# Kernel optimization log

Measured on AMD Instinct MI355X. Metric: run time of the kernel, lower is better.

## Reference

```python
import jax, jax.numpy as jnp
import numpy as np

D, H, K, L, F, G, M, OUT = 1280, 16, 80, 4, 5120, 48, 2, 2048
HALF = K // 2  # rotary half dim = 40


def _token_coords(grid_thw, merge_size, N):
    tpi = grid_thw[:, 0] * grid_thw[:, 1] * grid_thw[:, 2]
    cu = jnp.concatenate([jnp.zeros(1, jnp.int32), jnp.cumsum(tpi).astype(jnp.int32)])
    tok = jnp.arange(N, dtype=jnp.int32)
    img_id = jnp.searchsorted(cu[1:], tok, side='right')
    local = tok - cu[img_id]
    h = grid_thw[img_id, 1]
    w = grid_thw[img_id, 2]
    spatial = local % (h * w)
    msq = merge_size * merge_size
    mw = w // merge_size
    group, intra = spatial // msq, spatial % msq
    row = (group // mw) * merge_size + intra // merge_size
    col = (group % mw) * merge_size + intra % merge_size
    return row, col, h, w, cu


def _layernorm(x, s, b, eps=1e-6):
    mu = jnp.mean(x, -1, keepdims=True)
    var = jnp.mean(jnp.square(x - mu), -1, keepdims=True)
    return (x - mu) * jax.lax.rsqrt(var + eps) * s + b


def _rotate_half(x):
    x1, x2 = x[..., :HALF], x[..., HALF:]
    return jnp.concatenate([-x2, x1], axis=-1)


def setup_inputs() -> dict:
    key = jax.random.key(0)
    ks = jax.random.split(key, 16)
    s = 0.02
    inp = {
        'pixels': jax.random.normal(ks[0], (2048, 1536), jnp.float32),
        'grid_thw': jnp.array([[1, 16, 32]] * 4, jnp.int32),
        'pos_embed': jax.random.normal(ks[1], (G * G, D), jnp.float32) * s,
        'patch_w': jax.random.normal(ks[2], (1536, D), jnp.float32) * s,
        'patch_b': jnp.zeros((D,), jnp.float32),
        'ln1_s': jnp.ones((L, D), jnp.float32), 'ln1_b': jnp.zeros((L, D), jnp.float32),
        'qkv_w': jax.random.normal(ks[3], (L, D, 3 * D), jnp.float32) * s,
        'qkv_b': jnp.zeros((L, 3 * D), jnp.float32),
        'proj_w': jax.random.normal(ks[4], (L, D, D), jnp.float32) * s,
        'proj_b': jnp.zeros((L, D), jnp.float32),
        'ln2_s': jnp.ones((L, D), jnp.float32), 'ln2_b': jnp.zeros((L, D), jnp.float32),
        'fc1_w': jax.random.normal(ks[5], (L, D, F), jnp.float32) * s,
        'fc1_b': jnp.zeros((L, F), jnp.float32),
        'fc2_w': jax.random.normal(ks[6], (L, F, D), jnp.float32) * s,
        'fc2_b': jnp.zeros((L, D), jnp.float32),
        'm_norm_s': jnp.ones((D,), jnp.float32), 'm_norm_b': jnp.zeros((D,), jnp.float32),
        'm_fc1_w': jax.random.normal(ks[7], (D * M * M, D * M * M), jnp.float32) * s,
        'm_fc1_b': jnp.zeros((D * M * M,), jnp.float32),
        'm_fc2_w': jax.random.normal(ks[8], (D * M * M, OUT), jnp.float32) * s,
        'm_fc2_b': jnp.zeros((OUT,), jnp.float32),
    }
    return inp


def _forward(pixels, grid_thw, pos_embed, patch_w, patch_b, ln1_s, ln1_b, qkv_w, qkv_b,
             proj_w, proj_b, ln2_s, ln2_b, fc1_w, fc1_b, fc2_w, fc2_b,
             m_norm_s, m_norm_b, m_fc1_w, m_fc1_b, m_fc2_w, m_fc2_b):
    N = pixels.shape[0]
    row, col, h, w, cu = _token_coords(grid_thw, M, N)

    # patch embed: conv with stride==kernel over flattened patches == linear
    x = pixels @ patch_w + patch_b  # [N, D]

    # bilinear position-embedding interpolation onto each image's (h, w) grid
    rf = jnp.where(h > 1, row.astype(jnp.float32) * (G - 1) / jnp.maximum(h - 1, 1), 0.0)
    cf = jnp.where(w > 1, col.astype(jnp.float32) * (G - 1) / jnp.maximum(w - 1, 1), 0.0)
    r0 = jnp.floor(rf).astype(jnp.int32); r1 = jnp.minimum(r0 + 1, G - 1)
    c0 = jnp.floor(cf).astype(jnp.int32); c1 = jnp.minimum(c0 + 1, G - 1)
    wr = (rf - r0)[:, None]; wc = (cf - c0)[:, None]
    pe = (pos_embed[r0 * G + c0] * (1 - wr) * (1 - wc)
          + pos_embed[r0 * G + c1] * (1 - wr) * wc
          + pos_embed[r1 * G + c0] * wr * (1 - wc)
          + pos_embed[r1 * G + c1] * wr * wc)
    x = x + pe

    # 2-D rotary embeddings
    inv_freq = 1.0 / (10000.0 ** (jnp.arange(0, HALF, 2, dtype=jnp.float32) / HALF))
    freqs = jnp.concatenate([row[:, None].astype(jnp.float32) * inv_freq,
                             col[:, None].astype(jnp.float32) * inv_freq], axis=-1)  # [N, HALF]
    emb = jnp.concatenate([freqs, freqs], axis=-1)  # [N, K]
    cos, sin = jnp.cos(emb)[:, None, :], jnp.sin(emb)[:, None, :]  # [N,1,K]

    # block-diagonal segment mask via cu_seqlens (N is a multiple of 128; no pad)
    tok = jnp.arange(N)
    seg = jnp.searchsorted(cu[1:], tok, side='right')
    k_start = cu[jnp.minimum(seg, cu.shape[0] - 2)]
    k_end = cu[jnp.minimum(seg + 1, cu.shape[0] - 1)]
    mask = (tok[None, :] >= k_start[:, None]) & (tok[None, :] < k_end[:, None])  # [N,N]
    scale = K ** -0.5

    for l in range(L):
        hdn = _layernorm(x, ln1_s[l], ln1_b[l])
        qkv = (hdn @ qkv_w[l] + qkv_b[l]).reshape(N, 3, H, K)
        q, k, v = qkv[:, 0], qkv[:, 1], qkv[:, 2]
        q = q * cos + _rotate_half(q) * sin
        k = k * cos + _rotate_half(k) * sin
        scores = jnp.einsum('nhk,mhk->hnm', q, k) * scale
        scores = jnp.where(mask[None], scores, jnp.finfo(scores.dtype).min)
        attn = jax.nn.softmax(scores, axis=-1)
        o = jnp.einsum('hnm,mhk->nhk', attn, v).reshape(N, D)
        x = x + o @ proj_w[l] + proj_b[l]

        hdn = _layernorm(x, ln2_s[l], ln2_b[l])
        ff = jax.nn.gelu(hdn @ fc1_w[l] + fc1_b[l], approximate=True)
        x = x + ff @ fc2_w[l] + fc2_b[l]

    # patch merger
    normed = _layernorm(x, m_norm_s, m_norm_b).reshape(N // (M * M), D * M * M)
    ff = jax.nn.gelu(normed @ m_fc1_w + m_fc1_b, approximate=True)
    return ff @ m_fc2_w + m_fc2_b  # [N/4, OUT]


def reference(pixels, grid_thw, pos_embed, patch_w, patch_b, ln1_s, ln1_b, qkv_w, qkv_b,
              proj_w, proj_b, ln2_s, ln2_b, fc1_w, fc1_b, fc2_w, fc2_b,
              m_norm_s, m_norm_b, m_fc1_w, m_fc1_b, m_fc2_w, m_fc2_b):
    return _forward(pixels, grid_thw, pos_embed, patch_w, patch_b, ln1_s, ln1_b, qkv_w, qkv_b,
                    proj_w, proj_b, ln2_s, ln2_b, fc1_w, fc1_b, fc2_w, fc2_b,
                    m_norm_s, m_norm_b, m_fc1_w, m_fc1_b, m_fc2_w, m_fc2_b)
```

## Files before the change

kernel.cpp:

```cpp
#include <hip/hip_runtime.h>
#include <math.h>

#define DMODEL 1280
#define NHEADS 16
#define FDIM   5120
#define GPOS   48
#define SEG    512

typedef __attribute__((ext_vector_type(8))) short bf16x8;
typedef __attribute__((ext_vector_type(4))) float f32x4;
typedef unsigned short u16;

__device__ __forceinline__ u16 f2bf(float f) {
  unsigned int u = __float_as_uint(f);
  u = (u + 0x7FFFu + ((u >> 16) & 1u)) >> 16;
  return (u16)u;
}
__device__ __forceinline__ float bf2f(u16 u) {
  return __uint_as_float((unsigned int)u << 16);
}
__device__ __forceinline__ float gelu_tanh(float x) {
  float u = 0.7978845608028654f * (x + 0.044715f * x * x * x);
  float t = __expf(2.f * u);
  float th = 1.f - 2.f / (t + 1.f);
  return 0.5f * x * (1.f + th);
}

typedef const __attribute__((address_space(1))) unsigned int* gas_t;
typedef __attribute__((address_space(3))) unsigned int* las_t;
__device__ __forceinline__ void async16(const void* g, void* l) {
  __builtin_amdgcn_global_load_lds((gas_t)g, (las_t)l, 16, 0, 0);
}

#define STG256(mat, PW, ldx, h, kk, pp)                          \
  do {                                                           \
    const u16* g_ = (PW) + (long long)(h) * 128 * (ldx) + (kk);  \
    async16(g_, &L[pp][mat][h][(w * 2 + 0) * 512]);              \
    async16(g_ + 32, &L[pp][mat][h][(w * 2 + 1) * 512]);         \
  } while (0)

#define MM256(ii, ff)                                                          \
  acc[ii][ff] = __builtin_amdgcn_mfma_f32_16x16x32_bf16(aR[(ii) & 3][0],       \
                    bR[ff][0], acc[ii][ff], 0, 0, 0);                          \
  acc[ii][ff] = __builtin_amdgcn_mfma_f32_16x16x32_bf16(aR[(ii) & 3][1],       \
                    bR[ff][1], acc[ii][ff], 0, 0, 0);

#define BAR256() asm volatile("s_barrier" ::: "memory")
#define LGKM0() asm volatile("s_waitcnt lgkmcnt(0)" ::: "memory")

template <int EPI>
__global__ __launch_bounds__(512, 2) void gemm256(
    const u16* __restrict__ A, const u16* __restrict__ B,
    const float* __restrict__ bias, void* __restrict__ Cv,
    int Kd, int lda, int ldb, int ldc, int nsplit, long long pstride) {
  __shared__ __align__(16) u16 L[2][2][2][8192];
  const int sp = blockIdx.z;
  const int Ks = Kd / nsplit;
  const int NT = Ks >> 6;
  const u16* Ab = A + (long long)sp * Ks;
  const u16* Bb = B + (long long)sp * Ks;
  const int m0 = blockIdx.x * 256, n0 = blockIdx.y * 256;
  const int t = threadIdx.x, ln = t & 63, w = t >> 6;
  const int wr = w >> 2, wc = w & 3;
  const int m16 = ln & 15, q = ln >> 4;
  const int r16 = ln >> 2;
  const int csw = (ln & 3) ^ ((ln >> 5) << 1);
  const int rbase = m16 * 32 + (q ^ ((m16 >> 3) << 1)) * 8;

  const u16* Aw = Ab + (long long)(m0 + w * 16 + r16) * lda + csw * 8;
  const u16* Bw = Bb + (long long)(n0 + w * 16 + r16) * ldb + csw * 8;

  f32x4 acc[8][4];
#pragma unroll
  for (int i = 0; i < 8; i++)
#pragma unroll
    for (int j = 0; j < 4; j++)
#pragma unroll
      for (int r = 0; r < 4; r++) acc[i][j][r] = 0.f;

  auto stageT = [&](int tt, int pp) {
    int kk = tt * 64;
    STG256(0, Aw, lda, 0, kk, pp);
    STG256(0, Aw, lda, 1, kk, pp);
    STG256(1, Bw, ldb, 0, kk, pp);
    STG256(1, Bw, ldb, 1, kk, pp);
  };

  stageT(0, 0);
  if (NT > 1) {
    stageT(1, 1);
    asm volatile("s_waitcnt vmcnt(8)" ::: "memory");
  } else {
    asm volatile("s_waitcnt vmcnt(0)" ::: "memory");
  }
  BAR256();

  const int wb = (wc & 1) * 4;
  for (int tt = 0; tt < NT; ++tt) {
    const int p = tt & 1;
    const u16* Abuf = &L[p][0][wr][0];
    const u16* Bbuf = &L[p][1][wc >> 1][0];
    bf16x8 aR[4][2], bR[4][2];

#pragma unroll
    for (int i = 0; i < 4; ++i) {
      aR[i][0] = *(const bf16x8*)(Abuf + (i * 2 + 0) * 512 + rbase);
      aR[i][1] = *(const bf16x8*)(Abuf + (i * 2 + 1) * 512 + rbase);
    }
#pragma unroll
    for (int fc = 0; fc < 2; ++fc) {
      bR[fc][0] = *(const bf16x8*)(Bbuf + ((wb + fc) * 2 + 0) * 512 + rbase);
      bR[fc][1] = *(const bf16x8*)(Bbuf + ((wb + fc) * 2 + 1) * 512 + rbase);
    }
    BAR256();
    LGKM0();
    __builtin_amdgcn_s_setprio(1);
#pragma unroll
    for (int i = 0; i < 4; ++i) { MM256(i, 0); MM256(i, 1); }
    __builtin_amdgcn_s_setprio(0);
    BAR256();

#pragma unroll
    for (int fc = 2; fc < 4; ++fc) {
      bR[fc][0] = *(const bf16x8*)(Bbuf + ((wb + fc) * 2 + 0) * 512 + rbase);
      bR[fc][1] = *(const bf16x8*)(Bbuf + ((wb + fc) * 2 + 1) * 512 + rbase);
    }
    BAR256();
    LGKM0();
    __builtin_amdgcn_s_setprio(1);
#pragma unroll
    for (int i = 0; i < 4; ++i) { MM256(i, 2); MM256(i, 3); }
    __builtin_amdgcn_s_setprio(0);
    BAR256();

#pragma unroll
    for (int i = 0; i < 4; ++i) {
      aR[i][0] = *(const bf16x8*)(Abuf + ((4 + i) * 2 + 0) * 512 + rbase);
      aR[i][1] = *(const bf16x8*)(Abuf + ((4 + i) * 2 + 1) * 512 + rbase);
    }
    if (tt + 2 < NT) {
      STG256(1, Bw, ldb, 0, (tt + 2) * 64, p);
      STG256(1, Bw, ldb, 1, (tt + 2) * 64, p);
    }
    BAR256();
    LGKM0();
    __builtin_amdgcn_s_setprio(1);
#pragma unroll
    for (int i = 0; i < 4; ++i) { MM256(4 + i, 2); MM256(4 + i, 3); }
    __builtin_amdgcn_s_setprio(0);
    BAR256();

    if (tt + 2 < NT) {
      STG256(0, Aw, lda, 0, (tt + 2) * 64, p);
      STG256(0, Aw, lda, 1, (tt + 2) * 64, p);
    }
    BAR256();
    __builtin_amdgcn_s_setprio(1);
#pragma unroll
    for (int i = 0; i < 4; ++i) { MM256(4 + i, 0); MM256(4 + i, 1); }
    __builtin_amdgcn_s_setprio(0);
    if (tt + 2 < NT)      asm volatile("s_waitcnt vmcnt(8)" ::: "memory");
    else if (tt + 1 < NT) asm volatile("s_waitcnt vmcnt(0)" ::: "memory");
    BAR256();
  }

#pragma unroll
  for (int fr = 0; fr < 8; fr++) {
#pragma unroll
    for (int r = 0; r < 4; r++) {
      int row = m0 + wr * 128 + fr * 16 + q * 4 + r;
      if (EPI == 0) {
        u16* Cp = (u16*)Cv + (long long)sp * pstride + (long long)row * ldc;
#pragma unroll
        for (int fc = 0; fc < 4; fc++)
          Cp[n0 + wc * 64 + fc * 16 + m16] = f2bf(acc[fr][fc][r]);
      } else if (EPI == 1) {
        u16* Cb = (u16*)Cv + (long long)row * ldc;
#pragma unroll
        for (int fc = 0; fc < 4; fc++) {
          int col = n0 + wc * 64 + fc * 16 + m16;
          Cb[col] = f2bf(acc[fr][fc][r] + bias[col]);
        }
      } else {
        u16* Cb = (u16*)Cv + (long long)row * ldc;
#pragma unroll
        for (int fc = 0; fc < 4; fc++) {
          int col = n0 + wc * 64 + fc * 16 + m16;
          Cb[col] = f2bf(gelu_tanh(acc[fr][fc][r] + bias[col]));
        }
      }
    }
  }
}

__global__ __launch_bounds__(256) void fattn_k(
    const u16* __restrict__ qr, const u16* __restrict__ kr,
    const u16* __restrict__ vpT, u16* __restrict__ o, int N, float iscale) {
  __shared__ __align__(16) u16 Ks[2][24][512];
  __shared__ __align__(16) u16 Vs[2][20][512];
  __shared__ __align__(16) u16 Ps[4][32 * 128];
  const int nseg = N >> 9;
  const int hb = blockIdx.y;
  const int h = hb / nseg, seg = hb - h * nseg;
  const int t = threadIdx.x, ln = t & 63, w = t >> 6;
  const int m16 = ln & 15, qh = ln >> 4;
  const int r4 = ln >> 2, gsw = (ln & 3) ^ ((ln >> 5) << 1);
  const int rbase = m16 * 32 + ((qh ^ ((m16 >> 3) << 1)) << 3);
  const long long hN = (long long)h * N;
  const int segbase = seg * SEG;
  const int q0 = segbase + blockIdx.x * 128 + w * 32;

  bf16x8 qf[2][3];
#pragma unroll
  for (int mi = 0; mi < 2; mi++)
#pragma unroll
    for (int ks = 0; ks < 3; ks++)
      qf[mi][ks] = *(const bf16x8*)&qr[(hN + q0 + mi * 16 + m16) * 96 + ks * 32 + qh * 8];

  f32x4 ao[2][5];
#pragma unroll
  for (int mi = 0; mi < 2; mi++)
#pragma unroll
    for (int df = 0; df < 5; df++)
#pragma unroll
      for (int r = 0; r < 4; r++) ao[mi][df][r] = 0.f;
  float m_[2][4], l_[2][4];
#pragma unroll
  for (int mi = 0; mi < 2; mi++)
#pragma unroll
    for (int r = 0; r < 4; r++) { m_[mi][r] = -1e30f; l_[mi][r] = 0.f; }

  auto stage = [&](int c, int pb) {
#pragma unroll
    for (int i = 0; i < 6; i++) {
      int sK = w * 6 + i, f = sK / 3, kg = sK - f * 3;
      async16(&kr[(hN + segbase + c * 128 + f * 16 + r4) * 96 + kg * 32 + gsw * 8],
              &Ks[pb][sK][0]);
    }
#pragma unroll
    for (int i = 0; i < 5; i++) {
      int sV = w * 5 + i, df = sV >> 2, kvg = sV & 3;
      async16(&vpT[((long long)hb * 128 + df * 16 + r4) * SEG + c * 128 + kvg * 32 + gsw * 8],
              &Vs[pb][sV][0]);
    }
  };

  stage(0, 0);
  u16* Pmy = &Ps[w][0];
  for (int c = 0; c < 4; c++) {
    const int pb = c & 1;
    __syncthreads();
    if (c < 3) stage(c + 1, pb ^ 1);

    f32x4 s[2][8];
#pragma unroll
    for (int mi = 0; mi < 2; mi++)
#pragma unroll
      for (int f = 0; f < 8; f++)
#pragma unroll
        for (int r = 0; r < 4; r++) s[mi][f][r] = 0.f;
#pragma unroll
    for (int ks = 0; ks < 3; ks++) {
#pragma unroll
      for (int f = 0; f < 8; f++) {
        bf16x8 kf = *(const bf16x8*)&Ks[pb][f * 3 + ks][rbase];
#pragma unroll
        for (int mi = 0; mi < 2; mi++)
          s[mi][f] = __builtin_amdgcn_mfma_f32_16x16x32_bf16(qf[mi][ks], kf, s[mi][f], 0, 0, 0);
      }
    }

#pragma unroll
    for (int mi = 0; mi < 2; mi++) {
#pragma unroll
      for (int r = 0; r < 4; r++) {
        float mx = s[mi][0][r];
#pragma unroll
        for (int f = 1; f < 8; f++) mx = fmaxf(mx, s[mi][f][r]);
        mx *= iscale;
#pragma unroll
        for (int o2 = 1; o2 <= 8; o2 <<= 1) mx = fmaxf(mx, __shfl_xor(mx, o2));
        float mn = fmaxf(m_[mi][r], mx);
        float corr = __expf(m_[mi][r] - mn);
        m_[mi][r] = mn;
        float rs = 0.f;
#pragma unroll
        for (int f = 0; f < 8; f++) {
          float p = __expf(s[mi][f][r] * iscale - mn);
          s[mi][f][r] = p;
          rs += p;
        }
#pragma unroll
        for (int o2 = 1; o2 <= 8; o2 <<= 1) rs += __shfl_xor(rs, o2);
        l_[mi][r] = l_[mi][r] * corr + rs;
#pragma unroll
        for (int df = 0; df < 5; df++) ao[mi][df][r] *= corr;
      }
    }

#pragma unroll
    for (int mi = 0; mi < 2; mi++) {
#pragma unroll
      for (int r = 0; r < 4; r++) {
        int qq = mi * 16 + qh * 4 + r;
        int base = qq * 128 + (m16 & 7);
        int ql = qq & 7;
#pragma unroll
        for (int f = 0; f < 8; f++) {
          int gr = (f * 2 + (m16 >> 3)) ^ ql;
          Pmy[base + gr * 8] = f2bf(s[mi][f][r]);
        }
      }
    }

#pragma unroll
    for (int ks = 0; ks < 4; ks++) {
      bf16x8 pf[2];
#pragma unroll
      for (int mi = 0; mi < 2; mi++)
        pf[mi] = *(const bf16x8*)&Pmy[(mi * 16 + m16) * 128 +
                                      (((ks * 4 + qh) ^ (m16 & 7)) << 3)];
#pragma unroll
      for (int df = 0; df < 5; df++) {
        bf16x8 vf = *(const bf16x8*)&Vs[pb][df * 4 + ks][rbase];
#pragma unroll
        for (int mi = 0; mi < 2; mi++)
          ao[mi][df] = __builtin_amdgcn_mfma_f32_16x16x32_bf16(pf[mi], vf, ao[mi][df], 0, 0, 0);
      }
    }
  }

#pragma unroll
  for (int mi = 0; mi < 2; mi++) {
#pragma unroll
    for (int r = 0; r < 4; r++) {
      float rl = 1.f / l_[mi][r];
      long long rowb = (long long)(q0 + mi * 16 + qh * 4 + r) * DMODEL + h * 80;
#pragma unroll
      for (int df = 0; df < 5; df++)
        o[rowb + df * 16 + m16] = f2bf(ao[mi][df][r] * rl);
    }
  }
}

template <int S, int RES, int GELU, int OUTBF>
__global__ void reduce_k(const u16* __restrict__ Pp, long long mn, int Nn,
                         const float* __restrict__ bias,
                         const float* __restrict__ res, void* __restrict__ out) {
  long long i = ((long long)blockIdx.x * 256 + threadIdx.x) * 4;
  if (i >= mn) return;
  float vx = 0.f, vy = 0.f, vz = 0.f, vw = 0.f;
#pragma unroll
  for (int s = 0; s < S; s++) {
    ushort4 u4 = *(const ushort4*)(Pp + (long long)s * mn + i);
    vx += bf2f(u4.x); vy += bf2f(u4.y); vz += bf2f(u4.z); vw += bf2f(u4.w);
  }
  int col = (int)(i % Nn);
  vx += bias[col]; vy += bias[col + 1]; vz += bias[col + 2]; vw += bias[col + 3];
  if (GELU) {
    vx = gelu_tanh(vx); vy = gelu_tanh(vy);
    vz = gelu_tanh(vz); vw = gelu_tanh(vw);
  }
  if (RES) {
    float4 r4 = *(const float4*)(res + i);
    vx += r4.x; vy += r4.y; vz += r4.z; vw += r4.w;
  }
  if (OUTBF) {
    ushort4 o; o.x = f2bf(vx); o.y = f2bf(vy); o.z = f2bf(vz); o.w = f2bf(vw);
    *(ushort4*)((u16*)out + i) = o;
  } else {
    float4 o; o.x = vx; o.y = vy; o.z = vz; o.w = vw;
    *(float4*)((float*)out + i) = o;
  }
}

template <int S>
__global__ void redln_k(const u16* __restrict__ Pp, long long mn,
                        const float* __restrict__ bias,
                        float* __restrict__ x,
                        const float* __restrict__ s, const float* __restrict__ b,
                        u16* __restrict__ h) {
  int row = blockIdx.x;
  int d = threadIdx.x * 4;
  long long base = (long long)row * DMODEL + d;
  float vx = 0.f, vy = 0.f, vz = 0.f, vw = 0.f;
#pragma unroll
  for (int si = 0; si < S; si++) {
    ushort4 u4 = *(const ushort4*)(Pp + (long long)si * mn + base);
    vx += bf2f(u4.x); vy += bf2f(u4.y); vz += bf2f(u4.z); vw += bf2f(u4.w);
  }
  vx += bias[d]; vy += bias[d + 1]; vz += bias[d + 2]; vw += bias[d + 3];
  float4 r4 = *(const float4*)(x + base);
  vx += r4.x; vy += r4.y; vz += r4.z; vw += r4.w;
  float4 xv; xv.x = vx; xv.y = vy; xv.z = vz; xv.w = vw;
  *(float4*)(x + base) = xv;
  float sum = vx + vy + vz + vw;
#pragma unroll
  for (int o = 32; o; o >>= 1) sum += __shfl_xor(sum, o);
  __shared__ float red[8];
  int wv = threadIdx.x >> 6, lnn = threadIdx.x & 63;
  if (lnn == 0) red[wv] = sum;
  __syncthreads();
  float mu = 0.f;
  for (int i = 0; i < 5; i++) mu += red[i];
  mu *= (1.f / DMODEL);
  float dx = vx - mu, dy = vy - mu, dz = vz - mu, dw = vw - mu;
  float s2 = dx * dx + dy * dy + dz * dz + dw * dw;
#pragma unroll
  for (int o = 32; o; o >>= 1) s2 += __shfl_xor(s2, o);
  __syncthreads();
  if (lnn == 0) red[wv] = s2;
  __syncthreads();
  float var = 0.f;
  for (int i = 0; i < 5; i++) var += red[i];
  var *= (1.f / DMODEL);
  float rs = rsqrtf(var + 1e-6f);
  ushort4 o4;
  o4.x = f2bf(dx * rs * s[d] + b[d]);
  o4.y = f2bf(dy * rs * s[d + 1] + b[d + 1]);
  o4.z = f2bf(dz * rs * s[d + 2] + b[d + 2]);
  o4.w = f2bf(dw * rs * s[d + 3] + b[d + 3]);
  *(ushort4*)(h + base) = o4;
}

__global__ void wconv_k(const float* __restrict__ in, u16* __restrict__ out,
                        int K, int N) {
  __shared__ float tl[32][33];
  int n0 = blockIdx.x * 32, k0 = blockIdx.y * 32;
  int t = threadIdx.x;
  int r = t >> 5, c = t & 31;
#pragma unroll
  for (int i = 0; i < 4; i++)
    tl[r + 8 * i][c] = in[(long long)(k0 + r + 8 * i) * N + n0 + c];
  __syncthreads();
  int n = t >> 4, kp = (t & 15) * 2;
#pragma unroll
  for (int i = 0; i < 2; i++) {
    ushort2 o;
    o.x = f2bf(tl[kp][n + 16 * i]);
    o.y = f2bf(tl[kp + 1][n + 16 * i]);
    *(ushort2*)&out[(long long)(n0 + n + 16 * i) * K + k0 + kp] = o;
  }
}

__global__ void conv_k(const float* __restrict__ in, u16* __restrict__ out,
                       long long n) {
  long long i = ((long long)blockIdx.x * 256 + threadIdx.x) * 4;
  if (i >= n) return;
  float4 v = *(const float4*)(in + i);
  ushort4 o; o.x = f2bf(v.x); o.y = f2bf(v.y); o.z = f2bf(v.z); o.w = f2bf(v.w);
  *(ushort4*)&out[i] = o;
}

union U16x8 { uint4 v; u16 s[8]; };
__global__ void vtr_k(const u16* __restrict__ in, u16* __restrict__ out) {
  __shared__ u16 tl[64][65];
  int b = blockIdx.z;
  int m0 = blockIdx.x * 64;
  int d0 = blockIdx.y * 64;
  const u16* ib = in + (long long)b * SEG * 128;
  u16* ob = out + (long long)b * 128 * SEG;
  int t = threadIdx.x;
  int r = t >> 3, c8 = (t & 7) * 8;
#pragma unroll
  for (int i = 0; i < 2; i++) {
    U16x8 ld;
    ld.v = *(const uint4*)&ib[(long long)(m0 + r + 32 * i) * 128 + d0 + c8];
#pragma unroll
    for (int j = 0; j < 8; j++) tl[r + 32 * i][c8 + j] = ld.s[j];
  }
  __syncthreads();
  int d = t >> 3, m8 = (t & 7) * 8;
#pragma unroll
  for (int i = 0; i < 2; i++) {
    int dd = d + 32 * i;
    U16x8 st;
#pragma unroll
    for (int j = 0; j < 8; j++) st.s[j] = tl[m8 + j][dd];
    *(uint4*)&ob[(long long)(d0 + dd) * SEG + m0 + m8] = st.v;
  }
}

__global__ void coords_k(const int* __restrict__ g, int nimg,
                         int* __restrict__ rw, int* __restrict__ cl,
                         int* __restrict__ hh, int* __restrict__ ww, int N) {
  int t = blockIdx.x * 256 + threadIdx.x;
  if (t >= N) return;
  int c = 0, local = 0, H = 1, W = 1;
  for (int i = 0; i < nimg; i++) {
    int tpi = g[i * 3] * g[i * 3 + 1] * g[i * 3 + 2];
    if (t >= c && t < c + tpi) { local = t - c; H = g[i * 3 + 1]; W = g[i * 3 + 2]; }
    c += tpi;
  }
  int hw = H * W;
  int sp = local % hw;
  int mw = W >> 1;
  int gr = sp >> 2, intra = sp & 3;
  rw[t] = (gr / mw) * 2 + (intra >> 1);
  cl[t] = (gr % mw) * 2 + (intra & 1);
  hh[t] = H; ww[t] = W;
}

__global__ void peadd_k(float* __restrict__ x, const float* __restrict__ pe,
                        const int* __restrict__ rw, const int* __restrict__ cl,
                        const int* __restrict__ hh, const int* __restrict__ ww) {
  int n = blockIdx.x;
  int d = threadIdx.x * 4;
  int H = hh[n], W = ww[n];
  float rf = (H > 1) ? (float)rw[n] * (float)(GPOS - 1) / (float)(H - 1) : 0.f;
  float cf = (W > 1) ? (float)cl[n] * (float)(GPOS - 1) / (float)(W - 1) : 0.f;
  int r0 = (int)floorf(rf), c0 = (int)floorf(cf);
  int r1 = min(r0 + 1, GPOS - 1), c1 = min(c0 + 1, GPOS - 1);
  float wr = rf - (float)r0, wc = cf - (float)c0;
  float w00 = (1.f - wr) * (1.f - wc), w01 = (1.f - wr) * wc;
  float w10 = wr * (1.f - wc), w11 = wr * wc;
  float4 v00 = *(const float4*)(pe + (long long)(r0 * GPOS + c0) * DMODEL + d);
  float4 v01 = *(const float4*)(pe + (long long)(r0 * GPOS + c1) * DMODEL + d);
  float4 v10 = *(const float4*)(pe + (long long)(r1 * GPOS + c0) * DMODEL + d);
  float4 v11 = *(const float4*)(pe + (long long)(r1 * GPOS + c1) * DMODEL + d);
  float4 xv = *(float4*)(x + (long long)n * DMODEL + d);
  xv.x += w00 * v00.x + w01 * v01.x + w10 * v10.x + w11 * v11.x;
  xv.y += w00 * v00.y + w01 * v01.y + w10 * v10.y + w11 * v11.y;
  xv.z += w00 * v00.z + w01 * v01.z + w10 * v10.z + w11 * v11.z;
  xv.w += w00 * v00.w + w01 * v01.w + w10 * v10.w + w11 * v11.w;
  *(float4*)(x + (long long)n * DMODEL + d) = xv;
}

__global__ void ln_k(const float* __restrict__ X, u16* __restrict__ Y,
                     const float* __restrict__ s, const float* __restrict__ b) {
  int row = blockIdx.x;
  int d = threadIdx.x * 4;
  const float* x = X + (long long)row * DMODEL;
  float4 v = *(const float4*)(x + d);
  float sum = v.x + v.y + v.z + v.w;
#pragma unroll
  for (int o = 32; o; o >>= 1) sum += __shfl_xor(sum, o);
  __shared__ float red[8];
  int wv = threadIdx.x >> 6, lnn = threadIdx.x & 63;
  if (lnn == 0) red[wv] = sum;
  __syncthreads();
  float mu = 0.f;
  for (int i = 0; i < 5; i++) mu += red[i];
  mu *= (1.f / DMODEL);
  float dx = v.x - mu, dy = v.y - mu, dz = v.z - mu, dw = v.w - mu;
  float s2 = dx * dx + dy * dy + dz * dz + dw * dw;
#pragma unroll
  for (int o = 32; o; o >>= 1) s2 += __shfl_xor(s2, o);
  __syncthreads();
  if (lnn == 0) red[wv] = s2;
  __syncthreads();
  float var = 0.f;
  for (int i = 0; i < 5; i++) var += red[i];
  var *= (1.f / DMODEL);
  float rs = rsqrtf(var + 1e-6f);
  ushort4 o4;
  o4.x = f2bf(dx * rs * s[d] + b[d]);
  o4.y = f2bf(dy * rs * s[d + 1] + b[d + 1]);
  o4.z = f2bf(dz * rs * s[d + 2] + b[d + 2]);
  o4.w = f2bf(dw * rs * s[d + 3] + b[d + 3]);
  *(ushort4*)(Y + (long long)row * DMODEL + d) = o4;
}

__global__ void rope_k(const u16* __restrict__ qkv, const int* __restrict__ rw,
                       const int* __restrict__ cl, u16* __restrict__ qr,
                       u16* __restrict__ kr, u16* __restrict__ vp, int N) {
  int n = blockIdx.x, h = blockIdx.y, t = threadIdx.x;
  const u16* src = qkv + (long long)n * (3 * DMODEL) + h * 80;
  long long ob96 = ((long long)h * N + n) * 96;
  long long ob128 = ((long long)h * N + n) * 128;
  if (t < 40) {
    float pos = (t < 20) ? (float)rw[n] : (float)cl[n];
    float infr = exp2f(-13.287712379549449f * (float)(t % 20) * 0.05f);
    float f = pos * infr;
    float cs = cosf(f), sn = sinf(f);
    float q0 = bf2f(src[t]), q1 = bf2f(src[t + 40]);
    qr[ob96 + t] = f2bf(q0 * cs - q1 * sn);
    qr[ob96 + t + 40] = f2bf(q1 * cs + q0 * sn);
    float k0 = bf2f(src[DMODEL + t]), k1 = bf2f(src[DMODEL + t + 40]);
    kr[ob96 + t] = f2bf(k0 * cs - k1 * sn);
    kr[ob96 + t + 40] = f2bf(k1 * cs + k0 * sn);
    vp[ob128 + t] = src[2 * DMODEL + t];
    vp[ob128 + t + 40] = src[2 * DMODEL + t + 40];
  } else {
    int u = t - 40;
    if (u < 16) { qr[ob96 + 80 + u] = 0; kr[ob96 + 80 + u] = 0; }
    vp[ob128 + 80 + u] = 0;
    vp[ob128 + 104 + u] = 0;
  }
}

static void gemm_big(hipStream_t st, int epi, const u16* A, const u16* B,
                     const float* bias, void* C, int M, int Nn, int Kd,
                     int lda, int ldb, int ldc, int nsplit) {
  dim3 g(M / 256, Nn / 256, nsplit), blk(512);
  long long ps = (long long)M * Nn;
  switch (epi) {
    case 0: gemm256<0><<<g, blk, 0, st>>>(A, B, bias, C, Kd, lda, ldb, ldc, nsplit, ps); break;
    case 1: gemm256<1><<<g, blk, 0, st>>>(A, B, bias, C, Kd, lda, ldb, ldc, nsplit, ps); break;
    default: gemm256<3><<<g, blk, 0, st>>>(A, B, bias, C, Kd, lda, ldb, ldc, nsplit, ps); break;
  }
}

extern "C" void kernel_launch(void* const* d_in, const int* in_sizes, int n_in,
                              void* d_out, int out_size, void* d_ws, size_t ws_size,
                              hipStream_t stream) {
  const float* pixels = (const float*)d_in[0];
  const int* grid_thw = (const int*)d_in[1];
  const float* pos_embed = (const float*)d_in[2];
  const float* patch_w = (const float*)d_in[3];
  const float* patch_b = (const float*)d_in[4];
  const float* ln1_s = (const float*)d_in[5];
  const float* ln1_b = (const float*)d_in[6];
  const float* qkv_w = (const float*)d_in[7];
  const float* qkv_b = (const float*)d_in[8];
  const float* proj_w = (const float*)d_in[9];
  const float* proj_b = (const float*)d_in[10];
  const float* ln2_s = (const float*)d_in[11];
  const float* ln2_b = (const float*)d_in[12];
  const float* fc1_w = (const float*)d_in[13];
  const float* fc1_b = (const float*)d_in[14];
  const float* fc2_w = (const float*)d_in[15];
  const float* fc2_b = (const float*)d_in[16];
  const float* mns = (const float*)d_in[17];
  const float* mnb = (const float*)d_in[18];
  const float* mf1w = (const float*)d_in[19];
  const float* mf1b = (const float*)d_in[20];
  const float* mf2w = (const float*)d_in[21];
  const float* mf2b = (const float*)d_in[22];
  float* out = (float*)d_out;

  const int N = in_sizes[0] / 1536;
  const int nimg = in_sizes[1] / 3;
  const int nseg = N / SEG;
  const int nb = NHEADS * nseg;

  char* w = (char*)d_ws;
  size_t off = 0;
  auto alloc = [&](size_t bytes) -> void* {
    void* p = w + off;
    off += (bytes + 255) & ~(size_t)255;
    return p;
  };
  int* rw = (int*)alloc((size_t)N * 4);
  int* cl = (int*)alloc((size_t)N * 4);
  int* hh = (int*)alloc((size_t)N * 4);
  int* ww = (int*)alloc((size_t)N * 4);
  float* x = (float*)alloc((size_t)N * DMODEL * 4);
  u16* h = (u16*)alloc((size_t)N * DMODEL * 2);
  u16* pixbf = (u16*)alloc((size_t)N * 1536 * 2);
  u16* patchT = (u16*)alloc((size_t)DMODEL * 1536 * 2);
  u16* qkvT = (u16*)alloc((size_t)3 * DMODEL * DMODEL * 2);
  u16* projT = (u16*)alloc((size_t)DMODEL * DMODEL * 2);
  u16* fc1T = (u16*)alloc((size_t)FDIM * DMODEL * 2);
  u16* fc2T = (u16*)alloc((size_t)DMODEL * FDIM * 2);
  u16* qkvb = (u16*)alloc((size_t)N * 3 * DMODEL * 2);
  u16* qr = (u16*)alloc((size_t)NHEADS * N * 96 * 2);
  u16* kr = (u16*)alloc((size_t)NHEADS * N * 96 * 2);
  u16* vp = (u16*)alloc((size_t)NHEADS * N * 128 * 2);
  u16* vpT = (u16*)alloc((size_t)NHEADS * N * 128 * 2);
  u16* pad0 = (u16*)alloc((size_t)nb * 2 * SEG * 128 * 2);
  u16* o = (u16*)alloc((size_t)N * DMODEL * 2);
  float* bigA = (float*)alloc((size_t)nb * SEG * SEG * 4);
  float* bigB = (float*)alloc((size_t)nb * SEG * SEG * 2);
  (void)ws_size; (void)pad0;
  u16* mfc1T = qkvb;
  u16* mfc2T = pixbf;
  u16* ffb = (u16*)bigA;
  u16* mf = (u16*)bigA;
  u16* part = (u16*)bigB;

  const float iscale = 0.11180339887498949f;
  const long long mnD = (long long)N * DMODEL;

  coords_k<<<dim3((N + 255) / 256), 256, 0, stream>>>(grid_thw, nimg, rw, cl, hh, ww, N);
  conv_k<<<dim3((int)(((long long)N * 1536 / 4 + 255) / 256)), 256, 0, stream>>>(
      pixels, pixbf, (long long)N * 1536);
  wconv_k<<<dim3(DMODEL / 32, 1536 / 32), 256, 0, stream>>>(patch_w, patchT, 1536, DMODEL);
  gemm_big(stream, 0, pixbf, patchT, nullptr, part, N, DMODEL, 1536, 1536, 1536,
           DMODEL, 4);
  reduce_k<4, 0, 0, 0><<<dim3((int)((mnD / 4 + 255) / 256)), 256, 0, stream>>>(
      part, mnD, DMODEL, patch_b, nullptr, x);
  peadd_k<<<dim3(N), 320, 0, stream>>>(x, pos_embed, rw, cl, hh, ww);
  ln_k<<<dim3(N), 320, 0, stream>>>(x, h, ln1_s, ln1_b);

  for (int l = 0; l < 4; l++) {
    wconv_k<<<dim3(3 * DMODEL / 32, DMODEL / 32), 256, 0, stream>>>(
        qkv_w + (size_t)l * DMODEL * 3 * DMODEL, qkvT, DMODEL, 3 * DMODEL);
    wconv_k<<<dim3(DMODEL / 32, DMODEL / 32), 256, 0, stream>>>(
        proj_w + (size_t)l * DMODEL * DMODEL, projT, DMODEL, DMODEL);
    wconv_k<<<dim3(FDIM / 32, DMODEL / 32), 256, 0, stream>>>(
        fc1_w + (size_t)l * DMODEL * FDIM, fc1T, DMODEL, FDIM);
    wconv_k<<<dim3(DMODEL / 32, FDIM / 32), 256, 0, stream>>>(
        fc2_w + (size_t)l * FDIM * DMODEL, fc2T, FDIM, DMODEL);

    gemm_big(stream, 1, h, qkvT, qkv_b + (size_t)l * 3 * DMODEL, qkvb, N,
             3 * DMODEL, DMODEL, DMODEL, DMODEL, 3 * DMODEL, 1);
    rope_k<<<dim3(N, NHEADS), 64, 0, stream>>>(qkvb, rw, cl, qr, kr, vp, N);
    vtr_k<<<dim3(8, 2, nb), 256, 0, stream>>>(vp, vpT);
    fattn_k<<<dim3(SEG / 128, nb), 256, 0, stream>>>(qr, kr, vpT, o, N, iscale);
    gemm_big(stream, 0, o, projT, nullptr, part, N, DMODEL, DMODEL, DMODEL,
             DMODEL, DMODEL, 4);
    redln_k<4><<<dim3(N), 320, 0, stream>>>(part, mnD, proj_b + (size_t)l * DMODEL,
                                            x, ln2_s + (size_t)l * DMODEL,
                                            ln2_b + (size_t)l * DMODEL, h);
    gemm_big(stream, 3, h, fc1T, fc1_b + (size_t)l * FDIM, ffb, N, FDIM, DMODEL,
             DMODEL, DMODEL, FDIM, 1);
    gemm_big(stream, 0, ffb, fc2T, nullptr, part, N, DMODEL, FDIM, FDIM, FDIM,
             DMODEL, 4);
    const float* nsl = (l < 3) ? ln1_s + (size_t)(l + 1) * DMODEL : mns;
    const float* nbl = (l < 3) ? ln1_b + (size_t)(l + 1) * DMODEL : mnb;
    redln_k<4><<<dim3(N), 320, 0, stream>>>(part, mnD, fc2_b + (size_t)l * DMODEL,
                                            x, nsl, nbl, h);
  }

  const int Mm = N / 4;
  wconv_k<<<dim3(FDIM / 32, FDIM / 32), 256, 0, stream>>>(mf1w, mfc1T, FDIM, FDIM);
  gemm_big(stream, 0, h, mfc1T, nullptr, part, Mm, FDIM, FDIM, FDIM, FDIM, FDIM, 4);
  reduce_k<4, 0, 1, 1><<<dim3((int)(((long long)Mm * FDIM / 4 + 255) / 256)), 256, 0, stream>>>(
      part, (long long)Mm * FDIM, FDIM, mf1b, nullptr, mf);
  wconv_k<<<dim3(2048 / 32, FDIM / 32), 256, 0, stream>>>(mf2w, mfc2T, FDIM, 2048);
  gemm_big(stream, 0, mf, mfc2T, nullptr, part, Mm, 2048, FDIM, FDIM, FDIM, 2048, 16);
  reduce_k<16, 0, 0, 0><<<dim3((int)(((long long)Mm * 2048 / 4 + 255) / 256)), 256, 0, stream>>>(
      part, (long long)Mm * 2048, 2048, mf2b, nullptr, out);
}
```

Baseline: 1.506 ms.

## Restagger GEMM global prefetch and apply split-K to QKV, FC1 and merger GEMMs

The GEMM main loop now issues the next tile's A loads one step ahead, interleaved with the LDS reads, and spreads the B loads two steps ahead across phases. This is meant to even out outstanding memory traffic and hide latency behind the MFMA blocks. On the host side, the QKV and FC1 GEMMs switch from fused epilogues to split-K 2 plus a reduce kernel, FC2 and merger FC1 go to split-K 8, and a second partials buffer is carved from bigA. These changes add more blocks for occupancy, at the cost of extra reduce passes, more partial-sum memory traffic and a risk of the partA region overlapping with ffb.

```diff
diff --git a/kernel.cpp b/kernel.cpp
--- a/kernel.cpp
+++ b/kernel.cpp
@@ -78,18 +78,14 @@
 #pragma unroll
       for (int r = 0; r < 4; r++) acc[i][j][r] = 0.f;
 
-  auto stageT = [&](int tt, int pp) {
-    int kk = tt * 64;
-    STG256(0, Aw, lda, 0, kk, pp);
-    STG256(0, Aw, lda, 1, kk, pp);
-    STG256(1, Bw, ldb, 0, kk, pp);
-    STG256(1, Bw, ldb, 1, kk, pp);
-  };
-
-  stageT(0, 0);
+  STG256(0, Aw, lda, 0, 0, 0);
+  STG256(0, Aw, lda, 1, 0, 0);
+  STG256(1, Bw, ldb, 0, 0, 0);
+  STG256(1, Bw, ldb, 1, 0, 0);
   if (NT > 1) {
-    stageT(1, 1);
-    asm volatile("s_waitcnt vmcnt(8)" ::: "memory");
+    STG256(1, Bw, ldb, 0, 64, 1);
+    STG256(1, Bw, ldb, 1, 64, 1);
+    asm volatile("s_waitcnt vmcnt(4)" ::: "memory");
   } else {
     asm volatile("s_waitcnt vmcnt(0)" ::: "memory");
   }
@@ -112,6 +108,7 @@
       bR[fc][0] = *(const bf16x8*)(Bbuf + ((wb + fc) * 2 + 0) * 512 + rbase);
       bR[fc][1] = *(const bf16x8*)(Bbuf + ((wb + fc) * 2 + 1) * 512 + rbase);
     }
+    if (tt + 1 < NT) STG256(0, Aw, lda, 0, (tt + 1) * 64, (tt + 1) & 1);
     BAR256();
     LGKM0();
     __builtin_amdgcn_s_setprio(1);
@@ -125,6 +122,7 @@
       bR[fc][0] = *(const bf16x8*)(Bbuf + ((wb + fc) * 2 + 0) * 512 + rbase);
       bR[fc][1] = *(const bf16x8*)(Bbuf + ((wb + fc) * 2 + 1) * 512 + rbase);
     }
+    if (tt + 1 < NT) STG256(0, Aw, lda, 1, (tt + 1) * 64, (tt + 1) & 1);
     BAR256();
     LGKM0();
     __builtin_amdgcn_s_setprio(1);
@@ -138,10 +136,7 @@
       aR[i][0] = *(const bf16x8*)(Abuf + ((4 + i) * 2 + 0) * 512 + rbase);
       aR[i][1] = *(const bf16x8*)(Abuf + ((4 + i) * 2 + 1) * 512 + rbase);
     }
-    if (tt + 2 < NT) {
-      STG256(1, Bw, ldb, 0, (tt + 2) * 64, p);
-      STG256(1, Bw, ldb, 1, (tt + 2) * 64, p);
-    }
+    if (tt + 2 < NT) STG256(1, Bw, ldb, 0, (tt + 2) * 64, p);
     BAR256();
     LGKM0();
     __builtin_amdgcn_s_setprio(1);
@@ -150,17 +145,17 @@
     __builtin_amdgcn_s_setprio(0);
     BAR256();
 
-    if (tt + 2 < NT) {
-      STG256(0, Aw, lda, 0, (tt + 2) * 64, p);
-      STG256(0, Aw, lda, 1, (tt + 2) * 64, p);
-    }
+    if (tt + 2 < NT) STG256(1, Bw, ldb, 1, (tt + 2) * 64, p);
     BAR256();
+    LGKM0();
     __builtin_amdgcn_s_setprio(1);
 #pragma unroll
     for (int i = 0; i < 4; ++i) { MM256(4 + i, 0); MM256(4 + i, 1); }
     __builtin_amdgcn_s_setprio(0);
-    if (tt + 2 < NT)      asm volatile("s_waitcnt vmcnt(8)" ::: "memory");
-    else if (tt + 1 < NT) asm volatile("s_waitcnt vmcnt(0)" ::: "memory");
+    if (tt + 1 < NT) {
+      if (tt + 2 < NT) asm volatile("s_waitcnt vmcnt(4)" ::: "memory");
+      else             asm volatile("s_waitcnt vmcnt(0)" ::: "memory");
+    }
     BAR256();
   }
 
@@ -668,6 +663,7 @@
   u16* ffb = (u16*)bigA;
   u16* mf = (u16*)bigA;
   u16* part = (u16*)bigB;
+  u16* partA = (u16*)bigA + (size_t)11 * 1024 * 1024;
 
   const float iscale = 0.11180339887498949f;
   const long long mnD = (long long)N * DMODEL;
@@ -693,8 +689,11 @@
     wconv_k<<<dim3(DMODEL / 32, FDIM / 32), 256, 0, stream>>>(
         fc2_w + (size_t)l * FDIM * DMODEL, fc2T, FDIM, DMODEL);
 
-    gemm_big(stream, 1, h, qkvT, qkv_b + (size_t)l * 3 * DMODEL, qkvb, N,
-             3 * DMODEL, DMODEL, DMODEL, DMODEL, 3 * DMODEL, 1);
+    gemm_big(stream, 0, h, qkvT, nullptr, part, N, 3 * DMODEL, DMODEL,
+             DMODEL, DMODEL, 3 * DMODEL, 2);
+    reduce_k<2, 0, 0, 1><<<dim3((int)(((long long)N * 3 * DMODEL / 4 + 255) / 256)), 256, 0, stream>>>(
+        part, (long long)N * 3 * DMODEL, 3 * DMODEL,
+        qkv_b + (size_t)l * 3 * DMODEL, nullptr, qkvb);
     rope_k<<<dim3(N, NHEADS), 64, 0, stream>>>(qkvb, rw, cl, qr, kr, vp, N);
     vtr_k<<<dim3(8, 2, nb), 256, 0, stream>>>(vp, vpT);
     fattn_k<<<dim3(SEG / 128, nb), 256, 0, stream>>>(qr, kr, vpT, o, N, iscale);
@@ -703,21 +702,23 @@
     redln_k<4><<<dim3(N), 320, 0, stream>>>(part, mnD, proj_b + (size_t)l * DMODEL,
                                             x, ln2_s + (size_t)l * DMODEL,
                                             ln2_b + (size_t)l * DMODEL, h);
-    gemm_big(stream, 3, h, fc1T, fc1_b + (size_t)l * FDIM, ffb, N, FDIM, DMODEL,
-             DMODEL, DMODEL, FDIM, 1);
-    gemm_big(stream, 0, ffb, fc2T, nullptr, part, N, DMODEL, FDIM, FDIM, FDIM,
-             DMODEL, 4);
+    gemm_big(stream, 0, h, fc1T, nullptr, partA, N, FDIM, DMODEL,
+             DMODEL, DMODEL, FDIM, 2);
+    reduce_k<2, 0, 1, 1><<<dim3((int)(((long long)N * FDIM / 4 + 255) / 256)), 256, 0, stream>>>(
+        partA, (long long)N * FDIM, FDIM, fc1_b + (size_t)l * FDIM, nullptr, ffb);
+    gemm_big(stream, 0, ffb, fc2T, nullptr, partA, N, DMODEL, FDIM, FDIM, FDIM,
+             DMODEL, 8);
     const float* nsl = (l < 3) ? ln1_s + (size_t)(l + 1) * DMODEL : mns;
     const float* nbl = (l < 3) ? ln1_b + (size_t)(l + 1) * DMODEL : mnb;
-    redln_k<4><<<dim3(N), 320, 0, stream>>>(part, mnD, fc2_b + (size_t)l * DMODEL,
+    redln_k<8><<<dim3(N), 320, 0, stream>>>(partA, mnD, fc2_b + (size_t)l * DMODEL,
                                             x, nsl, nbl, h);
   }
 
   const int Mm = N / 4;
   wconv_k<<<dim3(FDIM / 32, FDIM / 32), 256, 0, stream>>>(mf1w, mfc1T, FDIM, FDIM);
-  gemm_big(stream, 0, h, mfc1T, nullptr, part, Mm, FDIM, FDIM, FDIM, FDIM, FDIM, 4);
-  reduce_k<4, 0, 1, 1><<<dim3((int)(((long long)Mm * FDIM / 4 + 255) / 256)), 256, 0, stream>>>(
-      part, (long long)Mm * FDIM, FDIM, mf1b, nullptr, mf);
+  gemm_big(stream, 0, h, mfc1T, nullptr, partA, Mm, FDIM, FDIM, FDIM, FDIM, FDIM, 8);
+  reduce_k<8, 0, 1, 1><<<dim3((int)(((long long)Mm * FDIM / 4 + 255) / 256)), 256, 0, stream>>>(
+      partA, (long long)Mm * FDIM, FDIM, mf1b, nullptr, mf);
   wconv_k<<<dim3(2048 / 32, FDIM / 32), 256, 0, stream>>>(mf2w, mfc2T, FDIM, 2048);
   gemm_big(stream, 0, mf, mfc2T, nullptr, part, Mm, 2048, FDIM, FDIM, FDIM, 2048, 16);
   reduce_k<16, 0, 0, 0><<<dim3((int)(((long long)Mm * 2048 / 4 + 255) / 256)), 256, 0, stream>>>(
```

Measured after the change: 1.518 ms. No clear change (+0.8%).
